# Optimization experiments

Measured on AMD Instinct MI355X. Metric: run time of the kernel, lower is better.

## Reference

```python
import jax, jax.numpy as jnp
import numpy as np

NUM_HEADS = 16
HEAD_DIM = 64
LN_EPS = 1e-12


def _interleave_pairs(a, b):
    # stack([a, b], -1).reshape(..., 2*d) -> interleaved on last dim
    return jnp.stack([a, b], axis=-1).reshape(a.shape[:-1] + (a.shape[-1] * 2,))


def _rotate_half(x):
    # stack([-x[..., 1::2], x[..., ::2]], -1).reshape_as(x)
    return _interleave_pairs(-x[..., 1::2], x[..., ::2])


def setup_inputs() -> dict:
    key = jax.random.key(0)
    ks = jax.random.split(key, 4)
    B, S, H = 4, 2048, 1024
    hidden_states = jax.random.normal(ks[0], (B, S, H), dtype=jnp.float32)
    sinusoidal_pos = jax.random.uniform(ks[1], (1, 1, S, HEAD_DIM), dtype=jnp.float32)
    ln_weight = jnp.ones((H,), dtype=jnp.float32)
    ln_bias = jnp.zeros((H,), dtype=jnp.float32)
    w_qkv = jax.random.normal(ks[2], (H, 3 * H), dtype=jnp.float32) * (1.0 / np.sqrt(H))
    b_qkv = jax.random.normal(ks[3], (3 * H,), dtype=jnp.float32) * 0.02
    return {"hidden_states": hidden_states, "sinusoidal_pos": sinusoidal_pos,
            "ln_weight": ln_weight, "ln_bias": ln_bias, "w_qkv": w_qkv, "b_qkv": b_qkv}


def reference(hidden_states, sinusoidal_pos, ln_weight, ln_bias, w_qkv, b_qkv):
    B, S, H = hidden_states.shape
    # LayerNorm
    mu = jnp.mean(hidden_states, axis=-1, keepdims=True)
    var = jnp.mean(jnp.square(hidden_states - mu), axis=-1, keepdims=True)
    h = (hidden_states - mu) * jax.lax.rsqrt(var + LN_EPS) * ln_weight + ln_bias
    # Fused QKV projection
    qkv = h @ w_qkv + b_qkv                       # [B, S, 3H]
    q, k, v = jnp.split(qkv, 3, axis=-1)
    def to_heads(x):
        return x.reshape(B, S, NUM_HEADS, HEAD_DIM).transpose(0, 2, 1, 3)  # [B, Hn, S, D]
    q, k, v = to_heads(q), to_heads(k), to_heads(v)
    # RoPE (RoFormer interleaved style)
    sin, cos = jnp.split(sinusoidal_pos, 2, axis=-1)      # each [1,1,S,D/2]
    sin_pos = _interleave_pairs(sin, sin)                 # [1,1,S,D]
    cos_pos = _interleave_pairs(cos, cos)
    q = q * cos_pos + _rotate_half(q) * sin_pos
    k = k * cos_pos + _rotate_half(k) * sin_pos
    # SDPA (non-causal, no mask, eval-mode dropout=0)
    scale = 1.0 / np.sqrt(HEAD_DIM)
    scores = jnp.einsum('bhqd,bhkd->bhqk', q, k) * scale
    probs = jax.nn.softmax(scores, axis=-1)
    ctx = jnp.einsum('bhqk,bhkd->bhqd', probs, v)         # [B, Hn, S, D]
    ctx = ctx.transpose(0, 2, 1, 3).reshape(B, S, H)
    return ctx
```

## Files before the change

kernel.cpp:

```cpp
#include <hip/hip_runtime.h>
#include <hip/hip_bf16.h>
#include <cstdint>
#include <cstddef>

#define DEVINL __device__ __forceinline__

typedef float f32x4 __attribute__((ext_vector_type(4)));
typedef float f32x16 __attribute__((ext_vector_type(16)));
typedef short s16x8 __attribute__((ext_vector_type(8)));
typedef short s16x4 __attribute__((ext_vector_type(4)));

static constexpr int Sd = 2048;
static constexpr int Hd = 1024;
static constexpr int NHd = 16;
static constexpr int Dd = 64;
static constexpr int N3 = 3072;

DEVINL float bf2f(short u){
  unsigned int t = ((unsigned int)(unsigned short)u) << 16;
  float f; __builtin_memcpy(&f, &t, 4); return f;
}
DEVINL short f2bf(float f){
  unsigned int t; __builtin_memcpy(&t, &f, 4);
  unsigned int r = t + 0x7FFFu + ((t >> 16) & 1u);
  return (short)(r >> 16);
}

DEVINL void gld16(const short* g, short* l){
  __builtin_amdgcn_global_load_lds((const __attribute__((address_space(1))) unsigned int*)g,
                                   (__attribute__((address_space(3))) unsigned int*)l, 16, 0, 0);
}

DEVINL int cvtpk(float lo, float hi){
  int r; asm("v_cvt_pk_bf16_f32 %0, %1, %2" : "=v"(r) : "v"(lo), "v"(hi)); return r;
}

DEVINL float fexp2(float x){
#if __has_builtin(__builtin_amdgcn_exp2f)
  return __builtin_amdgcn_exp2f(x);
#else
  return exp2f(x);
#endif
}

DEVINL f32x16 z16(){
  f32x16 v;
  #pragma unroll
  for (int i=0;i<16;i++) v[i]=0.f;
  return v;
}

__global__ __launch_bounds__(256) void ln_kernel(const float* __restrict__ x,
                                                 const float* __restrict__ w,
                                                 const float* __restrict__ bs,
                                                 short* __restrict__ h){
  int row = blockIdx.x, tid = threadIdx.x;
  const float* xr = x + (size_t)row * Hd;
  f32x4 v = *(const f32x4*)(xr + tid*4);
  float s1 = v[0]+v[1]+v[2]+v[3];
  float s2 = v[0]*v[0]+v[1]*v[1]+v[2]*v[2]+v[3]*v[3];
  #pragma unroll
  for (int off = 1; off < 64; off <<= 1){ s1 += __shfl_xor(s1, off); s2 += __shfl_xor(s2, off); }
  __shared__ float red[8];
  if ((tid & 63) == 0){ red[(tid>>6)*2] = s1; red[(tid>>6)*2+1] = s2; }
  __syncthreads();
  s1 = red[0]+red[2]+red[4]+red[6];
  s2 = red[1]+red[3]+red[5]+red[7];
  float mu = s1 * (1.0f/Hd);
  float rstd = rsqrtf(s2*(1.0f/Hd) - mu*mu + 1e-12f);
  f32x4 wv = *(const f32x4*)(w + tid*4);
  f32x4 bv = *(const f32x4*)(bs + tid*4);
  s16x4 o;
  #pragma unroll
  for (int i=0;i<4;i++) o[i] = f2bf((v[i]-mu)*rstd*wv[i] + bv[i]);
  *(s16x4*)(h + (size_t)row*Hd + tid*4) = o;
}

__global__ __launch_bounds__(256) void castw_kernel(const float* __restrict__ w, short* __restrict__ wT){
  __shared__ float t[32][33];
  int n0 = blockIdx.x*32, k0 = blockIdx.y*32;
  int tx = threadIdx.x, ty = threadIdx.y;
  #pragma unroll
  for (int i=0;i<4;i++) t[ty + i*8][tx] = w[(size_t)(k0 + ty + i*8)*N3 + n0 + tx];
  __syncthreads();
  #pragma unroll
  for (int i=0;i<4;i++) wT[(size_t)(n0 + ty + i*8)*Hd + k0 + tx] = f2bf(t[tx][ty + i*8]);
}

__global__ __launch_bounds__(256) void gemm_kernel(const short* __restrict__ A,
                                                   const short* __restrict__ Bt,
                                                   const float* __restrict__ bias,
                                                   short* __restrict__ qo,
                                                   short* __restrict__ ko,
                                                   short* __restrict__ vo){
  __shared__ short lA[128*32];
  __shared__ short lB[128*32];
  int bid = blockIdx.x;
  int xcd = bid & 7, idx = bid >> 3;
  int mt = xcd*8 + (idx & 7), nt = idx >> 3;
  int m0 = mt*128, n0 = nt*128;
  int tid = threadIdx.x, lane = tid & 63, wv = tid >> 6;
  int l15 = lane & 15, lq = lane >> 4;
  int wr = wv >> 1, wc = wv & 1;
  f32x4 zero = {0.f,0.f,0.f,0.f};
  f32x4 acc[4][4];
  #pragma unroll
  for (int m=0;m<4;m++)
    #pragma unroll
    for (int n=0;n<4;n++) acc[m][n] = zero;
  int flat = tid*8;
  int row0 = flat >> 5, col0 = flat & 31;
  const short* ga = A  + (size_t)(m0 + row0)*Hd + col0;
  const short* gb = Bt + (size_t)(n0 + row0)*Hd + col0;
  short* lAw = lA + wv*512;
  short* lBw = lB + wv*512;
  for (int kk = 0; kk < Hd; kk += 32){
    __syncthreads();
    gld16(ga + kk,                 lAw);
    gld16(ga + kk + (size_t)64*Hd, lAw + 2048);
    gld16(gb + kk,                 lBw);
    gld16(gb + kk + (size_t)64*Hd, lBw + 2048);
    __syncthreads();
    s16x8 af[4], bf[4];
    #pragma unroll
    for (int m=0;m<4;m++) af[m] = *(const s16x8*)(lA + (wr*64 + m*16 + l15)*32 + 8*lq);
    #pragma unroll
    for (int n=0;n<4;n++) bf[n] = *(const s16x8*)(lB + (wc*64 + n*16 + l15)*32 + 8*lq);
    #pragma unroll
    for (int m=0;m<4;m++)
      #pragma unroll
      for (int n=0;n<4;n++)
        acc[m][n] = __builtin_amdgcn_mfma_f32_16x16x32_bf16(af[m], bf[n], acc[m][n], 0, 0, 0);
  }
  #pragma unroll
  for (int n=0;n<4;n++){
    int c = n0 + wc*64 + n*16 + l15;
    float bv = bias[c];
    int part = c >> 10, hh = (c >> 6) & 15, d = c & 63;
    short* dst = part == 0 ? qo : (part == 1 ? ko : vo);
    #pragma unroll
    for (int m=0;m<4;m++){
      #pragma unroll
      for (int j=0;j<4;j++){
        int r = m0 + wr*64 + m*16 + lq*4 + j;
        int b = r >> 11, s = r & 2047;
        dst[(((size_t)((b*NHd + hh)*Sd + s)) << 6) + d] = f2bf(acc[m][n][j] + bv);
      }
    }
  }
}

__global__ __launch_bounds__(256) void prep_kernel(short* __restrict__ k,
                                                   const short* __restrict__ v,
                                                   short* __restrict__ vT,
                                                   const float* __restrict__ sp){
  if (blockIdx.y == 0){
    unsigned int idx = blockIdx.x*256 + threadIdx.x;
    unsigned int r = idx >> 2;
    int quarter = idx & 3;
    int s = r & 2047;
    short* p = k + ((size_t)r << 6) + quarter*16;
    s16x8 x0 = *(s16x8*)(p), x1 = *(s16x8*)(p + 8);
    const float* sr = sp + (size_t)s*64 + quarter*8;
    f32x4 sn0 = *(const f32x4*)(sr),      sn1 = *(const f32x4*)(sr + 4);
    f32x4 cs0 = *(const f32x4*)(sr + 32), cs1 = *(const f32x4*)(sr + 36);
    s16x8 y0, y1;
    #pragma unroll
    for (int j=0;j<4;j++){
      float e = bf2f(x0[2*j]), o = bf2f(x0[2*j+1]);
      y0[2*j]   = f2bf(e*cs0[j] - o*sn0[j]);
      y0[2*j+1] = f2bf(o*cs0[j] + e*sn0[j]);
      float e1 = bf2f(x1[2*j]), o1 = bf2f(x1[2*j+1]);
      y1[2*j]   = f2bf(e1*cs1[j] - o1*sn1[j]);
      y1[2*j+1] = f2bf(o1*cs1[j] + e1*sn1[j]);
    }
    *(s16x8*)(p) = y0; *(s16x8*)(p + 8) = y1;
  } else {
    __shared__ short t[64*65];
    int s0 = (blockIdx.x & 31)*64, bh = blockIdx.x >> 5;
    int tid = threadIdx.x;
    int srow = tid >> 2, cb = (tid & 3) * 16;
    const short* src = v + (((size_t)bh*Sd + s0 + srow) << 6) + cb;
    s16x8 a = *(const s16x8*)(src), b = *(const s16x8*)(src + 8);
    #pragma unroll
    for (int j=0;j<8;j++){ t[(cb+j)*65 + srow] = a[j]; t[(cb+8+j)*65 + srow] = b[j]; }
    __syncthreads();
    int d = tid >> 2, sb = (tid & 3) * 16;
    s16x8 o0, o1;
    #pragma unroll
    for (int j=0;j<8;j++){ o0[j] = t[d*65 + sb + j]; o1[j] = t[d*65 + sb + 8 + j]; }
    size_t obase = (((size_t)bh*Dd + d) << 11) + s0 + sb;
    *(s16x8*)(vT + obase)     = o0;
    *(s16x8*)(vT + obase + 8) = o1;
  }
}

__global__ __launch_bounds__(512, 4) void attn_kernel(const short* __restrict__ q,
                                                      const short* __restrict__ k,
                                                      const short* __restrict__ vT,
                                                      const float* __restrict__ sp,
                                                      float* __restrict__ out){
  __shared__ alignas(16) short kbuf[2][8192];
  __shared__ alignas(16) short vbuf[2][8192];
  int bid = blockIdx.x;
  int xcd = bid & 7, w = bid >> 3;
  int bh = xcd*8 + (w >> 3), qb = w & 7;
  int tid = threadIdx.x, lane = tid & 63, wv = tid >> 6;
  int l31 = lane & 31, hi = lane >> 5;
  const short* kp = k  + ((size_t)bh << 17);
  const short* vp = vT + ((size_t)bh << 17);
  int qrow = qb*256 + wv*32 + l31;
  const short* qp = q + ((size_t)bh << 17) + (size_t)qrow*64;
  const float* spq = sp + (size_t)qrow*64;
  const float qs = 0.18033688011112042f;
  s16x8 qf[4];
  #pragma unroll
  for (int kk=0;kk<4;kk++){
    s16x8 x = *(const s16x8*)(qp + kk*16 + hi*8);
    f32x4 sn = *(const f32x4*)(spq + kk*8 + hi*4);
    f32x4 cs = *(const f32x4*)(spq + 32 + kk*8 + hi*4);
    s16x8 y;
    #pragma unroll
    for (int j=0;j<4;j++){
      float e = bf2f(x[2*j]), o = bf2f(x[2*j+1]);
      y[2*j]   = f2bf((e*cs[j] - o*sn[j])*qs);
      y[2*j+1] = f2bf((o*cs[j] + e*sn[j])*qs);
    }
    qf[kk] = y;
  }
  int kc0 = tid,      kr0 = kc0 >> 3;
  int kc1 = tid+512,  kr1 = kc1 >> 3;
  int koff0 = kr0*64 + ((kc0 ^ kr0) & 7)*8;
  int koff1 = kr1*64 + ((kc1 ^ kr1) & 7)*8;
  int vr0 = tid >> 4,       vcc0 = tid & 15;
  int vr1 = (tid+512) >> 4, vcc1 = (tid+512) & 15;
  int voff0 = vr0*2048 + ((vcc0 & 8) | ((vcc0 ^ vr0) & 7))*8;
  int voff1 = vr1*2048 + ((vcc1 & 8) | ((vcc1 ^ vr1) & 7))*8;

  f32x16 ot0 = z16(), ot1 = z16();
  float m = -1e30f, lr = 0.f;
  int rsw = (l31 & 7);

#define STAGE(nb, t) do { \
    gld16(kp + (size_t)(t)*8192 + koff0, &kbuf[nb][0]    + wv*512); \
    gld16(kp + (size_t)(t)*8192 + koff1, &kbuf[nb][4096] + wv*512); \
    gld16(vp + (size_t)(t)*128  + voff0, &vbuf[nb][0]    + wv*512); \
    gld16(vp + (size_t)(t)*128  + voff1, &vbuf[nb][4096] + wv*512); \
  } while(0)

  STAGE(0, 0);
  __syncthreads();

  for (int t = 0; t < 16; ++t){
    int cur = t & 1;
    if (t < 15) STAGE(cur^1, t+1);
    #pragma unroll
    for (int h = 0; h < 2; ++h){
      const short* kb = &kbuf[cur][h*4096];
      const short* vb = &vbuf[cur][h*64];
      f32x16 s0 = z16(), s1 = z16();
      __builtin_amdgcn_s_setprio(1);
      #pragma unroll
      for (int kk=0;kk<4;kk++){
        s16x8 kf0 = *(const s16x8*)(kb + l31*64       + (((kk*2 + hi) ^ rsw)*8));
        s0 = __builtin_amdgcn_mfma_f32_32x32x16_bf16(kf0, qf[kk], s0, 0, 0, 0);
        s16x8 kf1 = *(const s16x8*)(kb + (32+l31)*64  + (((kk*2 + hi) ^ rsw)*8));
        s1 = __builtin_amdgcn_mfma_f32_32x32x16_bf16(kf1, qf[kk], s1, 0, 0, 0);
      }
      __builtin_amdgcn_s_setprio(0);
      float tm[16];
      #pragma unroll
      for (int i=0;i<16;i++) tm[i] = fmaxf(s0[i], s1[i]);
      #pragma unroll
      for (int off=8; off>=1; off>>=1)
        #pragma unroll
        for (int i=0;i<off;i++) tm[i] = fmaxf(tm[i], tm[i+off]);
      float pmax = fmaxf(tm[0], __shfl_xor(tm[0], 32));
      if (!__all(pmax - m <= 8.0f)){
        float mn = fmaxf(m, pmax);
        float al = fexp2(m - mn);
        m = mn; lr *= al;
        #pragma unroll
        for (int i=0;i<16;i++){ ot0[i] *= al; ot1[i] *= al; }
      }
      #pragma unroll
      for (int i=0;i<16;i++){ s0[i] = fexp2(s0[i]-m); s1[i] = fexp2(s1[i]-m); }
      float ra[16];
      #pragma unroll
      for (int i=0;i<16;i++) ra[i] = s0[i] + s1[i];
      #pragma unroll
      for (int off=8; off>=1; off>>=1)
        #pragma unroll
        for (int i=0;i<off;i++) ra[i] += ra[i+off];
      lr += ra[0] + __shfl_xor(ra[0], 32);
      #pragma unroll
      for (int s4=0;s4<4;s4++){
        int base = (s4 & 1) * 8;
        int pkA0, pkA1, pkB0, pkB1;
        if (s4 < 2){
          pkA0 = cvtpk(s0[base],   s0[base+1]); pkA1 = cvtpk(s0[base+2], s0[base+3]);
          pkB0 = cvtpk(s0[base+4], s0[base+5]); pkB1 = cvtpk(s0[base+6], s0[base+7]);
        } else {
          pkA0 = cvtpk(s1[base],   s1[base+1]); pkA1 = cvtpk(s1[base+2], s1[base+3]);
          pkB0 = cvtpk(s1[base+4], s1[base+5]); pkB1 = cvtpk(s1[base+6], s1[base+7]);
        }
        int r0 = __shfl_xor(hi ? pkA0 : pkB0, 32);
        int r1 = __shfl_xor(hi ? pkA1 : pkB1, 32);
        union { int wq[4]; s16x8 v8; } u;
        u.wq[0] = hi ? r0   : pkA0;
        u.wq[1] = hi ? r1   : pkA1;
        u.wq[2] = hi ? pkB0 : r0;
        u.wq[3] = hi ? pkB1 : r1;
        __builtin_amdgcn_s_setprio(1);
        s16x8 vf0 = *(const s16x8*)(vb + l31*128      + (((s4*2 + hi) ^ rsw)*8));
        ot0 = __builtin_amdgcn_mfma_f32_32x32x16_bf16(vf0, u.v8, ot0, 0, 0, 0);
        s16x8 vf1 = *(const s16x8*)(vb + (32+l31)*128 + (((s4*2 + hi) ^ rsw)*8));
        ot1 = __builtin_amdgcn_mfma_f32_32x32x16_bf16(vf1, u.v8, ot1, 0, 0, 0);
        __builtin_amdgcn_s_setprio(0);
      }
    }
    __syncthreads();
  }
#undef STAGE
  float inv = 1.0f / lr;
  int b = bh >> 4, hh = bh & 15;
  float* orow = out + ((size_t)(b*Sd + qrow) << 10) + hh*64;
  #pragma unroll
  for (int g=0; g<4; ++g){
    f32x4 w0, w1;
    #pragma unroll
    for (int j=0;j<4;j++){ w0[j] = ot0[4*g+j]*inv; w1[j] = ot1[4*g+j]*inv; }
    *(f32x4*)(orow + g*8 + 4*hi)      = w0;
    *(f32x4*)(orow + 32 + g*8 + 4*hi) = w1;
  }
}

extern "C" void kernel_launch(void* const* d_in, const int* in_sizes, int n_in,
                              void* d_out, int out_size, void* d_ws, size_t ws_size,
                              hipStream_t stream){
  const float* hs = (const float*)d_in[0];
  const float* sp = (const float*)d_in[1];
  const float* lw = (const float*)d_in[2];
  const float* lb = (const float*)d_in[3];
  const float* wq = (const float*)d_in[4];
  const float* bq = (const float*)d_in[5];
  float* out = (float*)d_out;
  char* ws = (char*)d_ws;
  short* h   = (short*)(ws);
  short* wT  = (short*)(ws + 16777216);
  short* vTb = (short*)(ws);
  short* qb_ = (short*)(ws + 23068672);
  short* kb_ = (short*)(ws + 23068672 + 16777216);
  short* vb_ = (short*)(ws + 23068672 + 33554432);

  hipLaunchKernelGGL(ln_kernel,    dim3(8192),    dim3(256),   0, stream, hs, lw, lb, h);
  hipLaunchKernelGGL(castw_kernel, dim3(96,32),   dim3(32,8),  0, stream, wq, wT);
  hipLaunchKernelGGL(gemm_kernel,  dim3(1536),    dim3(256),   0, stream, h, wT, bq, qb_, kb_, vb_);
  hipLaunchKernelGGL(prep_kernel,  dim3(2048,2),  dim3(256),   0, stream, kb_, vb_, vTb, sp);
  hipLaunchKernelGGL(attn_kernel,  dim3(512),     dim3(512),   0, stream, qb_, kb_, vTb, sp, out);
}
```

Baseline: 185.5 us.

## Fuse RoPE and V transpose into QKV GEMM epilogue, drop prep kernel

The GEMM epilogue now applies RoPE to Q and K, and folds the softmax scale into Q. It gets each pair partner with a lane xor-shuffle and reads sin/cos from the positional table. V is written directly in transposed [bh, d, s] layout with 4-wide stores. This removes the separate prep kernel, its extra round trip of K and V through global memory, and the Q RoPE work in the attention prologue. The cost is a heavier epilogue with per-element sin/cos gathers and strided V stores.

```diff
diff --git a/kernel.cpp b/kernel.cpp
--- a/kernel.cpp
+++ b/kernel.cpp
@@ -90,6 +90,7 @@
 __global__ __launch_bounds__(256) void gemm_kernel(const short* __restrict__ A,
                                                    const short* __restrict__ Bt,
                                                    const float* __restrict__ bias,
+                                                   const float* __restrict__ sp,
                                                    short* __restrict__ qo,
                                                    short* __restrict__ ko,
                                                    short* __restrict__ vo){
@@ -137,68 +138,40 @@
     int c = n0 + wc*64 + n*16 + l15;
     float bv = bias[c];
     int part = c >> 10, hh = (c >> 6) & 15, d = c & 63;
-    short* dst = part == 0 ? qo : (part == 1 ? ko : vo);
-    #pragma unroll
-    for (int m=0;m<4;m++){
-      #pragma unroll
-      for (int j=0;j<4;j++){
-        int r = m0 + wr*64 + m*16 + lq*4 + j;
-        int b = r >> 11, s = r & 2047;
-        dst[(((size_t)((b*NHd + hh)*Sd + s)) << 6) + d] = f2bf(acc[m][n][j] + bv);
+    if (part < 2){
+      short* dst = part == 0 ? qo : ko;
+      float sgnmul = (d & 1) ? 1.0f : -1.0f;
+      float postscale = part == 0 ? 0.18033688011112042f : 1.0f;
+      #pragma unroll
+      for (int m=0;m<4;m++){
+        #pragma unroll
+        for (int j=0;j<4;j++){
+          int r = m0 + wr*64 + m*16 + lq*4 + j;
+          int b = r >> 11, s = r & 2047;
+          float x = acc[m][n][j] + bv;
+          float xp = __shfl_xor(x, 1);
+          const float* sr = sp + (size_t)s*64 + (d>>1);
+          float y = (x*sr[32] + sgnmul*xp*sr[0]) * postscale;
+          dst[(((size_t)((b*NHd + hh)*Sd + s)) << 6) + d] = f2bf(y);
+        }
+      }
+    } else {
+      #pragma unroll
+      for (int m=0;m<4;m++){
+        int r0 = m0 + wr*64 + m*16 + lq*4;
+        int b = r0 >> 11, s0r = r0 & 2047;
+        s16x4 o;
+        #pragma unroll
+        for (int j=0;j<4;j++) o[j] = f2bf(acc[m][n][j] + bv);
+        *(s16x4*)(vo + (((size_t)((b*NHd + hh)*Dd + d)) << 11) + s0r) = o;
       }
     }
-  }
-}
-
-__global__ __launch_bounds__(256) void prep_kernel(short* __restrict__ k,
-                                                   const short* __restrict__ v,
-                                                   short* __restrict__ vT,
-                                                   const float* __restrict__ sp){
-  if (blockIdx.y == 0){
-    unsigned int idx = blockIdx.x*256 + threadIdx.x;
-    unsigned int r = idx >> 2;
-    int quarter = idx & 3;
-    int s = r & 2047;
-    short* p = k + ((size_t)r << 6) + quarter*16;
-    s16x8 x0 = *(s16x8*)(p), x1 = *(s16x8*)(p + 8);
-    const float* sr = sp + (size_t)s*64 + quarter*8;
-    f32x4 sn0 = *(const f32x4*)(sr),      sn1 = *(const f32x4*)(sr + 4);
-    f32x4 cs0 = *(const f32x4*)(sr + 32), cs1 = *(const f32x4*)(sr + 36);
-    s16x8 y0, y1;
-    #pragma unroll
-    for (int j=0;j<4;j++){
-      float e = bf2f(x0[2*j]), o = bf2f(x0[2*j+1]);
-      y0[2*j]   = f2bf(e*cs0[j] - o*sn0[j]);
-      y0[2*j+1] = f2bf(o*cs0[j] + e*sn0[j]);
-      float e1 = bf2f(x1[2*j]), o1 = bf2f(x1[2*j+1]);
-      y1[2*j]   = f2bf(e1*cs1[j] - o1*sn1[j]);
-      y1[2*j+1] = f2bf(o1*cs1[j] + e1*sn1[j]);
-    }
-    *(s16x8*)(p) = y0; *(s16x8*)(p + 8) = y1;
-  } else {
-    __shared__ short t[64*65];
-    int s0 = (blockIdx.x & 31)*64, bh = blockIdx.x >> 5;
-    int tid = threadIdx.x;
-    int srow = tid >> 2, cb = (tid & 3) * 16;
-    const short* src = v + (((size_t)bh*Sd + s0 + srow) << 6) + cb;
-    s16x8 a = *(const s16x8*)(src), b = *(const s16x8*)(src + 8);
-    #pragma unroll
-    for (int j=0;j<8;j++){ t[(cb+j)*65 + srow] = a[j]; t[(cb+8+j)*65 + srow] = b[j]; }
-    __syncthreads();
-    int d = tid >> 2, sb = (tid & 3) * 16;
-    s16x8 o0, o1;
-    #pragma unroll
-    for (int j=0;j<8;j++){ o0[j] = t[d*65 + sb + j]; o1[j] = t[d*65 + sb + 8 + j]; }
-    size_t obase = (((size_t)bh*Dd + d) << 11) + s0 + sb;
-    *(s16x8*)(vT + obase)     = o0;
-    *(s16x8*)(vT + obase + 8) = o1;
   }
 }
 
 __global__ __launch_bounds__(512, 4) void attn_kernel(const short* __restrict__ q,
                                                       const short* __restrict__ k,
                                                       const short* __restrict__ vT,
-                                                      const float* __restrict__ sp,
                                                       float* __restrict__ out){
   __shared__ alignas(16) short kbuf[2][8192];
   __shared__ alignas(16) short vbuf[2][8192];
@@ -211,23 +184,9 @@
   const short* vp = vT + ((size_t)bh << 17);
   int qrow = qb*256 + wv*32 + l31;
   const short* qp = q + ((size_t)bh << 17) + (size_t)qrow*64;
-  const float* spq = sp + (size_t)qrow*64;
-  const float qs = 0.18033688011112042f;
   s16x8 qf[4];
   #pragma unroll
-  for (int kk=0;kk<4;kk++){
-    s16x8 x = *(const s16x8*)(qp + kk*16 + hi*8);
-    f32x4 sn = *(const f32x4*)(spq + kk*8 + hi*4);
-    f32x4 cs = *(const f32x4*)(spq + 32 + kk*8 + hi*4);
-    s16x8 y;
-    #pragma unroll
-    for (int j=0;j<4;j++){
-      float e = bf2f(x[2*j]), o = bf2f(x[2*j+1]);
-      y[2*j]   = f2bf((e*cs[j] - o*sn[j])*qs);
-      y[2*j+1] = f2bf((o*cs[j] + e*sn[j])*qs);
-    }
-    qf[kk] = y;
-  }
+  for (int kk=0;kk<4;kk++) qf[kk] = *(const s16x8*)(qp + kk*16 + hi*8);
   int kc0 = tid,      kr0 = kc0 >> 3;
   int kc1 = tid+512,  kr1 = kc1 >> 3;
   int koff0 = kr0*64 + ((kc0 ^ kr0) & 7)*8;
@@ -348,14 +307,12 @@
   char* ws = (char*)d_ws;
   short* h   = (short*)(ws);
   short* wT  = (short*)(ws + 16777216);
-  short* vTb = (short*)(ws);
   short* qb_ = (short*)(ws + 23068672);
   short* kb_ = (short*)(ws + 23068672 + 16777216);
-  short* vb_ = (short*)(ws + 23068672 + 33554432);
+  short* vTb = (short*)(ws + 23068672 + 33554432);
 
   hipLaunchKernelGGL(ln_kernel,    dim3(8192),    dim3(256),   0, stream, hs, lw, lb, h);
   hipLaunchKernelGGL(castw_kernel, dim3(96,32),   dim3(32,8),  0, stream, wq, wT);
-  hipLaunchKernelGGL(gemm_kernel,  dim3(1536),    dim3(256),   0, stream, h, wT, bq, qb_, kb_, vb_);
-  hipLaunchKernelGGL(prep_kernel,  dim3(2048,2),  dim3(256),   0, stream, kb_, vb_, vTb, sp);
-  hipLaunchKernelGGL(attn_kernel,  dim3(512),     dim3(512),   0, stream, qb_, kb_, vTb, sp, out);
-}
+  hipLaunchKernelGGL(gemm_kernel,  dim3(1536),    dim3(256),   0, stream, h, wT, bq, sp, qb_, kb_, vTb);
+  hipLaunchKernelGGL(attn_kernel,  dim3(512),     dim3(512),   0, stream, qb_, kb_, vTb, out);
+}
```

Result: no change. 188.4 us (+1.6%).
